# Performance work log

Measured on AMD Instinct MI355X. Metric: run time of the kernel, lower is better.

The kernel has to match this reference:

```python
import jax, jax.numpy as jnp
import numpy as np

D_MODEL = 1024
N_HEADS = 16
HEAD_DIM = D_MODEL // N_HEADS
SCALE = HEAD_DIM ** -0.5  # 0.125


def setup_inputs() -> dict:
    key = jax.random.key(0)
    k1, k2, k3, k4 = jax.random.split(key, 4)
    B, H, S, d = 2, N_HEADS, 2048, HEAD_DIM
    q = jax.random.normal(k1, (B, H, S, d), dtype=jnp.float32)
    k = jax.random.normal(k2, (B, H, d, S), dtype=jnp.float32)  # pre-transposed, as in torch.matmul(q, k)
    v = jax.random.normal(k3, (B, H, S, d), dtype=jnp.float32)
    prev = jax.random.normal(k4, (B, H, S, S), dtype=jnp.float32)
    return {"q": q, "k": k, "v": v, "prev": prev}


def reference(q, k, v, prev):
    # attn_scores = (q @ k) * scale + prev   (scores must be returned pre-softmax)
    attn_scores = jnp.einsum("bhsd,bhdt->bhst", q, k) * SCALE + prev
    attn_weights = jax.nn.softmax(attn_scores, axis=-1)
    # dropout p=0.0 -> identity (module default / eval)
    out = jnp.einsum("bhst,bhtd->bhsd", attn_weights, v)
    return (out, attn_scores)
```

## Files before the change

kernel.cpp:

```cpp
#include <hip/hip_runtime.h>
#include <hip/hip_fp16.h>


typedef _Float16 half8 __attribute__((ext_vector_type(8)));
typedef _Float16 half4v __attribute__((ext_vector_type(4)));
typedef float f32x4 __attribute__((ext_vector_type(4)));

constexpr int S_LEN = 2048;
constexpr int DHEAD = 64;
constexpr int BH_TOT = 32;
constexpr float SCALE = 0.125f;
constexpr float LOG2E = 1.4426950408889634f;
constexpr float M_FIX = 8.0f * LOG2E;

__global__ __launch_bounds__(256) void tconv(const float* __restrict__ in,
                                             _Float16* __restrict__ outp,
                                             int R, int C) {
    const int head = blockIdx.z;
    const int r0 = blockIdx.y * 64, c0 = blockIdx.x * 64;
    const float* src = in + (size_t)head * R * C;
    _Float16* dst = outp + (size_t)head * R * C;
    __shared__ _Float16 t[64][68];
    const int tx = threadIdx.x & 63;
    const int ty = threadIdx.x >> 6;
    #pragma unroll
    for (int i = 0; i < 16; ++i) {
        const int rr = ty + i * 4;
        t[tx][rr] = (_Float16)src[(size_t)(r0 + rr) * C + c0 + tx];
    }
    __syncthreads();
    const int cw = threadIdx.x >> 4;
    const int dx = (threadIdx.x & 15) * 4;
    #pragma unroll
    for (int i = 0; i < 4; ++i) {
        const int crow = cw + i * 16;
        half4v vv;
        #pragma unroll
        for (int j = 0; j < 4; ++j) vv[j] = t[crow][dx + j];
        *reinterpret_cast<half4v*>(&dst[(size_t)(c0 + crow) * R + r0 + dx]) = vv;
    }
}

__global__ __launch_bounds__(512, 4) void attn_fused(
    const float* __restrict__ q, const float* __restrict__ prev,
    const _Float16* __restrict__ k16t, const _Float16* __restrict__ v16t,
    float* __restrict__ out, float* __restrict__ scores)
{
    const int lane = threadIdx.x & 63;
    const int wave = threadIdx.x >> 6;
    const int lg = lane >> 4;
    const int lr = lane & 15;

    const int bid = blockIdx.x;
    const int swz = (bid & 7) * 64 + (bid >> 3);
    const int bh = swz >> 4;
    const int rb = swz & 15;
    const int i0 = rb * 128 + wave * 16;

    const float* qh = q + (size_t)bh * S_LEN * DHEAD;
    const float* ph = prev + (size_t)bh * S_LEN * S_LEN;
    float* sh = scores + (size_t)bh * S_LEN * S_LEN;
    float* oh = out + (size_t)bh * S_LEN * DHEAD;
    const _Float16* kt = k16t + (size_t)bh * S_LEN * DHEAD;
    const _Float16* vt = v16t + (size_t)bh * S_LEN * DHEAD;

    __shared__ __align__(16) _Float16 sbuf[2][4096];
    __shared__ __align__(16) _Float16 p_lds[8][16][40];

    const _Float16* sbase;
    size_t slaneoff;
    int smul;
    if (wave < 4) {
        const int r = wave * 8 + (lane >> 3);
        slaneoff = (size_t)r * DHEAD + (size_t)((((lane & 7) ^ (r & 7)) * 8));
        smul = DHEAD;
        sbase = kt;
    } else {
        const int d = (wave - 4) * 16 + (lane >> 2);
        slaneoff = (size_t)d * S_LEN + (size_t)((((lane & 3) ^ ((d >> 1) & 3)) * 8));
        smul = 1;
        sbase = vt;
    }
    _Float16* const dstA = &sbuf[0][wave * 512 + lane * 8];
    _Float16* const dstB = &sbuf[1][wave * 512 + lane * 8];

    half8 qa[2];
    {
        const float* qrow = qh + (size_t)(i0 + lr) * DHEAD + lg * 8;
        #pragma unroll
        for (int h = 0; h < 2; ++h) {
            half8 t;
            #pragma unroll
            for (int e = 0; e < 8; ++e) t[e] = (_Float16)qrow[h * 32 + e];
            qa[h] = t;
        }
    }

    f32x4 acc[4] = {};
    float lsum[4] = {0.f, 0.f, 0.f, 0.f};

    auto load_prev = [&](int jt, float (&P)[8]) {
        #pragma unroll
        for (int r = 0; r < 4; ++r) {
            const size_t rowoff = (size_t)(i0 + lg * 4 + r) * S_LEN + jt + lr;
            P[r * 2]     = ph[rowoff];
            P[r * 2 + 1] = ph[rowoff + 16];
        }
    };

    half8 R;

    auto step = [&](int t, float (&P)[8]) {
        const int b = t & 1;
        *reinterpret_cast<half8*>(b ? dstA : dstB) = R;
        const int tn = (t + 2 < 64) ? t + 2 : 63;
        R = *reinterpret_cast<const half8*>(sbase + (size_t)(tn * 32) * smul + slaneoff);

        const _Float16* kB = &sbuf[b][0];
        half8 kb[4];
        #pragma unroll
        for (int s = 0; s < 2; ++s) {
            const int r = s * 16 + lr;
            #pragma unroll
            for (int h = 0; h < 2; ++h)
                kb[s * 2 + h] = *reinterpret_cast<const half8*>(
                    kB + r * 64 + (((h * 4 + lg) ^ (lr & 7)) * 8));
        }
        f32x4 sacc[2] = {};
        sacc[0] = __builtin_amdgcn_mfma_f32_16x16x32_f16(qa[0], kb[0], sacc[0], 0, 0, 0);
        sacc[0] = __builtin_amdgcn_mfma_f32_16x16x32_f16(qa[1], kb[1], sacc[0], 0, 0, 0);
        sacc[1] = __builtin_amdgcn_mfma_f32_16x16x32_f16(qa[0], kb[2], sacc[1], 0, 0, 0);
        sacc[1] = __builtin_amdgcn_mfma_f32_16x16x32_f16(qa[1], kb[3], sacc[1], 0, 0, 0);

        const int jt = t * 32;
        #pragma unroll
        for (int r = 0; r < 4; ++r) {
            const int row = lg * 4 + r;
            const size_t rowoff = (size_t)(i0 + row) * S_LEN + jt + lr;
            const float a0 = fmaf(sacc[0][r], SCALE, P[r * 2]);
            const float a1 = fmaf(sacc[1][r], SCALE, P[r * 2 + 1]);
            sh[rowoff] = a0;
            sh[rowoff + 16] = a1;
            const float p0 = exp2f(fmaf(a0, LOG2E, -M_FIX));
            const float p1 = exp2f(fmaf(a1, LOG2E, -M_FIX));
            lsum[r] += p0 + p1;
            p_lds[wave][row][lr]      = (_Float16)p0;
            p_lds[wave][row][lr + 16] = (_Float16)p1;
        }
        load_prev(tn * 32, P);

        const half8 pa = *reinterpret_cast<const half8*>(&p_lds[wave][lr][lg * 8]);
        #pragma unroll
        for (int f = 0; f < 4; ++f) {
            const int d = f * 16 + lr;
            const half8 vb = *reinterpret_cast<const half8*>(
                kB + 2048 + d * 32 + ((lg ^ ((lr >> 1) & 3)) * 8));
            acc[f] = __builtin_amdgcn_mfma_f32_16x16x32_f16(pa, vb, acc[f], 0, 0, 0);
        }

        asm volatile("s_waitcnt lgkmcnt(0)" ::: "memory");
        __builtin_amdgcn_s_barrier();
        asm volatile("" ::: "memory");
    };

    float PA[8], PB[8];
    R = *reinterpret_cast<const half8*>(sbase + slaneoff);
    *reinterpret_cast<half8*>(dstA) = R;
    R = *reinterpret_cast<const half8*>(sbase + (size_t)32 * smul + slaneoff);
    load_prev(0, PA);
    load_prev(32, PB);
    asm volatile("s_waitcnt lgkmcnt(0)" ::: "memory");
    __builtin_amdgcn_s_barrier();
    asm volatile("" ::: "memory");

    for (int t = 0; t < 64; t += 2) {
        step(t, PA);
        step(t + 1, PB);
    }

    #pragma unroll
    for (int r = 0; r < 4; ++r) {
        float s = lsum[r];
        s += __shfl_xor(s, 1);
        s += __shfl_xor(s, 2);
        s += __shfl_xor(s, 4);
        s += __shfl_xor(s, 8);
        const float inv = 1.0f / s;
        const size_t o = (size_t)(i0 + lg * 4 + r) * DHEAD + lr;
        #pragma unroll
        for (int f = 0; f < 4; ++f)
            oh[o + f * 16] = acc[f][r] * inv;
    }
}

__global__ __launch_bounds__(256, 4) void attn_fallback(
    const float* __restrict__ q, const float* __restrict__ k,
    const float* __restrict__ v, const float* __restrict__ prev,
    float* __restrict__ out, float* __restrict__ scores)
{
    const int lane = threadIdx.x & 63;
    const int wave = threadIdx.x >> 6;
    const int lg = lane >> 4, lr = lane & 15;
    const int bh = blockIdx.x >> 5;
    const int rowblk = blockIdx.x & 31;
    const int i0 = rowblk * 64 + wave * 16;

    const float* qh = q + (size_t)bh * S_LEN * DHEAD;
    const float* kh = k + (size_t)bh * DHEAD * S_LEN;
    const float* vh = v + (size_t)bh * S_LEN * DHEAD;
    const float* ph = prev + (size_t)bh * S_LEN * S_LEN;
    float* sh = scores + (size_t)bh * S_LEN * S_LEN;
    float* oh = out + (size_t)bh * S_LEN * DHEAD;

    __shared__ __align__(16) _Float16 p_lds[4][16][40];

    half8 qa[2];
    {
        const float* qrow = qh + (size_t)(i0 + lr) * DHEAD + lg * 8;
        #pragma unroll
        for (int h = 0; h < 2; ++h) {
            half8 t;
            #pragma unroll
            for (int e = 0; e < 8; ++e) t[e] = (_Float16)qrow[h * 32 + e];
            qa[h] = t;
        }
    }
    f32x4 acc[4] = {};
    float lsum[4] = {0.f, 0.f, 0.f, 0.f};

    for (int jt = 0; jt < S_LEN; jt += 32) {
        half8 kb[4], vb[4];
        #pragma unroll
        for (int h = 0; h < 2; ++h)
            #pragma unroll
            for (int s = 0; s < 2; ++s) {
                const float* kp = kh + (size_t)(h * 32 + lg * 8) * S_LEN + jt + s * 16 + lr;
                half8 t;
                #pragma unroll
                for (int e = 0; e < 8; ++e) t[e] = (_Float16)kp[(size_t)e * S_LEN];
                kb[s * 2 + h] = t;
            }
        #pragma unroll
        for (int f = 0; f < 4; ++f) {
            const float* vp = vh + (size_t)(jt + lg * 8) * DHEAD + f * 16 + lr;
            half8 t;
            #pragma unroll
            for (int e = 0; e < 8; ++e) t[e] = (_Float16)vp[(size_t)e * DHEAD];
            vb[f] = t;
        }
        f32x4 sacc[2] = {};
        sacc[0] = __builtin_amdgcn_mfma_f32_16x16x32_f16(qa[0], kb[0], sacc[0], 0, 0, 0);
        sacc[0] = __builtin_amdgcn_mfma_f32_16x16x32_f16(qa[1], kb[1], sacc[0], 0, 0, 0);
        sacc[1] = __builtin_amdgcn_mfma_f32_16x16x32_f16(qa[0], kb[2], sacc[1], 0, 0, 0);
        sacc[1] = __builtin_amdgcn_mfma_f32_16x16x32_f16(qa[1], kb[3], sacc[1], 0, 0, 0);
        #pragma unroll
        for (int r = 0; r < 4; ++r) {
            const size_t rowoff = (size_t)(i0 + lg * 4 + r) * S_LEN + jt + lr;
            const float a0 = fmaf(sacc[0][r], SCALE, ph[rowoff]);
            const float a1 = fmaf(sacc[1][r], SCALE, ph[rowoff + 16]);
            sh[rowoff] = a0;
            sh[rowoff + 16] = a1;
            const float p0 = exp2f(fmaf(a0, LOG2E, -M_FIX));
            const float p1 = exp2f(fmaf(a1, LOG2E, -M_FIX));
            lsum[r] += p0 + p1;
            p_lds[wave][lg * 4 + r][lr]      = (_Float16)p0;
            p_lds[wave][lg * 4 + r][lr + 16] = (_Float16)p1;
        }
        const half8 pa = *reinterpret_cast<const half8*>(&p_lds[wave][lr][lg * 8]);
        #pragma unroll
        for (int f = 0; f < 4; ++f)
            acc[f] = __builtin_amdgcn_mfma_f32_16x16x32_f16(pa, vb[f], acc[f], 0, 0, 0);
    }
    #pragma unroll
    for (int r = 0; r < 4; ++r) {
        float s = lsum[r];
        s += __shfl_xor(s, 1);
        s += __shfl_xor(s, 2);
        s += __shfl_xor(s, 4);
        s += __shfl_xor(s, 8);
        const float inv = 1.0f / s;
        const size_t o = (size_t)(i0 + lg * 4 + r) * DHEAD + lr;
        #pragma unroll
        for (int f = 0; f < 4; ++f)
            oh[o + f * 16] = acc[f][r] * inv;
    }
}

extern "C" void kernel_launch(void* const* d_in, const int* in_sizes, int n_in,
                              void* d_out, int out_size, void* d_ws, size_t ws_size,
                              hipStream_t stream) {
    const float* q    = (const float*)d_in[0];
    const float* k    = (const float*)d_in[1];
    const float* v    = (const float*)d_in[2];
    const float* prev = (const float*)d_in[3];
    float* out = (float*)d_out;
    float* scores = out + (size_t)BH_TOT * S_LEN * DHEAD;

    const size_t elems = (size_t)BH_TOT * S_LEN * DHEAD;
    const size_t need = 2 * elems * sizeof(_Float16);

    if (d_ws != nullptr && ws_size >= need) {
        _Float16* k16t = (_Float16*)d_ws;
        _Float16* v16t = k16t + elems;
        tconv<<<dim3(S_LEN / 64, DHEAD / 64, BH_TOT), 256, 0, stream>>>(k, k16t, DHEAD, S_LEN);
        tconv<<<dim3(DHEAD / 64, S_LEN / 64, BH_TOT), 256, 0, stream>>>(v, v16t, S_LEN, DHEAD);
        attn_fused<<<dim3(512), dim3(512), 0, stream>>>(q, prev, k16t, v16t, out, scores);
    } else {
        attn_fallback<<<dim3(1024), dim3(256), 0, stream>>>(q, k, v, prev, out, scores);
    }
}
```

Baseline: 310.7 us.

## Double key tile width to 64 columns per pipeline step

Widens each step's key/value tile from 32 to 64 columns, halving the number of steps and barriers. All 512 threads now stage both K and V tiles instead of splitting waves between them, and each thread prefetches 16 prev values instead of 8. This is meant to cut barrier and loop overhead per unit of work, at the cost of doubled LDS and more registers, which may lower occupancy under launch_bounds(512,4).

```diff
diff --git a/kernel.cpp b/kernel.cpp
--- a/kernel.cpp
+++ b/kernel.cpp
@@ -46,8 +46,9 @@
     const _Float16* __restrict__ k16t, const _Float16* __restrict__ v16t,
     float* __restrict__ out, float* __restrict__ scores)
 {
-    const int lane = threadIdx.x & 63;
-    const int wave = threadIdx.x >> 6;
+    const int tid = threadIdx.x;
+    const int lane = tid & 63;
+    const int wave = tid >> 6;
     const int lg = lane >> 4;
     const int lr = lane & 15;
 
@@ -64,25 +65,15 @@
     const _Float16* kt = k16t + (size_t)bh * S_LEN * DHEAD;
     const _Float16* vt = v16t + (size_t)bh * S_LEN * DHEAD;
 
-    __shared__ __align__(16) _Float16 sbuf[2][4096];
-    __shared__ __align__(16) _Float16 p_lds[8][16][40];
-
-    const _Float16* sbase;
-    size_t slaneoff;
-    int smul;
-    if (wave < 4) {
-        const int r = wave * 8 + (lane >> 3);
-        slaneoff = (size_t)r * DHEAD + (size_t)((((lane & 7) ^ (r & 7)) * 8));
-        smul = DHEAD;
-        sbase = kt;
-    } else {
-        const int d = (wave - 4) * 16 + (lane >> 2);
-        slaneoff = (size_t)d * S_LEN + (size_t)((((lane & 3) ^ ((d >> 1) & 3)) * 8));
-        smul = 1;
-        sbase = vt;
-    }
-    _Float16* const dstA = &sbuf[0][wave * 512 + lane * 8];
-    _Float16* const dstB = &sbuf[1][wave * 512 + lane * 8];
+    __shared__ __align__(16) _Float16 sbuf[2][8192];
+    __shared__ __align__(16) _Float16 p_lds[8][16][72];
+
+    const int sr = tid >> 3;
+    const int s8 = tid & 7;
+    const size_t srcKoff = (size_t)sr * DHEAD + (size_t)((s8 ^ (sr & 7)) * 8);
+    const size_t srcVoff = (size_t)sr * S_LEN + (size_t)((s8 ^ (sr & 7)) * 8);
+    _Float16* const dK[2] = {&sbuf[0][tid * 8], &sbuf[1][tid * 8]};
+    _Float16* const dV[2] = {&sbuf[0][4096 + tid * 8], &sbuf[1][4096 + tid * 8]};
 
     half8 qa[2];
     {
@@ -99,63 +90,63 @@
     f32x4 acc[4] = {};
     float lsum[4] = {0.f, 0.f, 0.f, 0.f};
 
-    auto load_prev = [&](int jt, float (&P)[8]) {
+    auto load_prev = [&](int jt, float (&P)[16]) {
         #pragma unroll
         for (int r = 0; r < 4; ++r) {
             const size_t rowoff = (size_t)(i0 + lg * 4 + r) * S_LEN + jt + lr;
-            P[r * 2]     = ph[rowoff];
-            P[r * 2 + 1] = ph[rowoff + 16];
+            #pragma unroll
+            for (int s = 0; s < 4; ++s)
+                P[r * 4 + s] = ph[rowoff + s * 16];
         }
     };
 
-    half8 R;
-
-    auto step = [&](int t, float (&P)[8]) {
+    half8 RK, RV;
+
+    auto step = [&](int t, float (&P)[16]) {
         const int b = t & 1;
-        *reinterpret_cast<half8*>(b ? dstA : dstB) = R;
-        const int tn = (t + 2 < 64) ? t + 2 : 63;
-        R = *reinterpret_cast<const half8*>(sbase + (size_t)(tn * 32) * smul + slaneoff);
+        *reinterpret_cast<half8*>(dK[b ^ 1]) = RK;
+        *reinterpret_cast<half8*>(dV[b ^ 1]) = RV;
+        const int tn = (t + 2 < 32) ? t + 2 : 31;
+        RK = *reinterpret_cast<const half8*>(kt + (size_t)(tn * 64) * DHEAD + srcKoff);
+        RV = *reinterpret_cast<const half8*>(vt + (size_t)(tn * 64) + srcVoff);
 
         const _Float16* kB = &sbuf[b][0];
-        half8 kb[4];
-        #pragma unroll
-        for (int s = 0; s < 2; ++s) {
+        const int jt = t * 64;
+
+        #pragma unroll
+        for (int s = 0; s < 4; ++s) {
             const int r = s * 16 + lr;
-            #pragma unroll
-            for (int h = 0; h < 2; ++h)
-                kb[s * 2 + h] = *reinterpret_cast<const half8*>(
+            f32x4 sacc = {};
+            #pragma unroll
+            for (int h = 0; h < 2; ++h) {
+                const half8 kb = *reinterpret_cast<const half8*>(
                     kB + r * 64 + (((h * 4 + lg) ^ (lr & 7)) * 8));
-        }
-        f32x4 sacc[2] = {};
-        sacc[0] = __builtin_amdgcn_mfma_f32_16x16x32_f16(qa[0], kb[0], sacc[0], 0, 0, 0);
-        sacc[0] = __builtin_amdgcn_mfma_f32_16x16x32_f16(qa[1], kb[1], sacc[0], 0, 0, 0);
-        sacc[1] = __builtin_amdgcn_mfma_f32_16x16x32_f16(qa[0], kb[2], sacc[1], 0, 0, 0);
-        sacc[1] = __builtin_amdgcn_mfma_f32_16x16x32_f16(qa[1], kb[3], sacc[1], 0, 0, 0);
-
-        const int jt = t * 32;
-        #pragma unroll
-        for (int r = 0; r < 4; ++r) {
-            const int row = lg * 4 + r;
-            const size_t rowoff = (size_t)(i0 + row) * S_LEN + jt + lr;
-            const float a0 = fmaf(sacc[0][r], SCALE, P[r * 2]);
-            const float a1 = fmaf(sacc[1][r], SCALE, P[r * 2 + 1]);
-            sh[rowoff] = a0;
-            sh[rowoff + 16] = a1;
-            const float p0 = exp2f(fmaf(a0, LOG2E, -M_FIX));
-            const float p1 = exp2f(fmaf(a1, LOG2E, -M_FIX));
-            lsum[r] += p0 + p1;
-            p_lds[wave][row][lr]      = (_Float16)p0;
-            p_lds[wave][row][lr + 16] = (_Float16)p1;
-        }
-        load_prev(tn * 32, P);
-
-        const half8 pa = *reinterpret_cast<const half8*>(&p_lds[wave][lr][lg * 8]);
-        #pragma unroll
-        for (int f = 0; f < 4; ++f) {
-            const int d = f * 16 + lr;
-            const half8 vb = *reinterpret_cast<const half8*>(
-                kB + 2048 + d * 32 + ((lg ^ ((lr >> 1) & 3)) * 8));
-            acc[f] = __builtin_amdgcn_mfma_f32_16x16x32_f16(pa, vb, acc[f], 0, 0, 0);
+                sacc = __builtin_amdgcn_mfma_f32_16x16x32_f16(qa[h], kb, sacc, 0, 0, 0);
+            }
+            #pragma unroll
+            for (int rr = 0; rr < 4; ++rr) {
+                const int row = lg * 4 + rr;
+                const float a = fmaf(sacc[rr], SCALE, P[rr * 4 + s]);
+                sh[(size_t)(i0 + row) * S_LEN + jt + s * 16 + lr] = a;
+                const float p = exp2f(fmaf(a, LOG2E, -M_FIX));
+                lsum[rr] += p;
+                p_lds[wave][row][s * 16 + lr] = (_Float16)p;
+            }
+        }
+
+        load_prev(tn * 64, P);
+
+        #pragma unroll
+        for (int ks = 0; ks < 2; ++ks) {
+            const half8 pa = *reinterpret_cast<const half8*>(
+                &p_lds[wave][lr][ks * 32 + lg * 8]);
+            #pragma unroll
+            for (int f = 0; f < 4; ++f) {
+                const int d = f * 16 + lr;
+                const half8 vb = *reinterpret_cast<const half8*>(
+                    kB + 4096 + d * 64 + (((ks * 4 + lg) ^ (lr & 7)) * 8));
+                acc[f] = __builtin_amdgcn_mfma_f32_16x16x32_f16(pa, vb, acc[f], 0, 0, 0);
+            }
         }
 
         asm volatile("s_waitcnt lgkmcnt(0)" ::: "memory");
@@ -163,17 +154,20 @@
         asm volatile("" ::: "memory");
     };
 
-    float PA[8], PB[8];
-    R = *reinterpret_cast<const half8*>(sbase + slaneoff);
-    *reinterpret_cast<half8*>(dstA) = R;
-    R = *reinterpret_cast<const half8*>(sbase + (size_t)32 * smul + slaneoff);
+    float PA[16], PB[16];
+    RK = *reinterpret_cast<const half8*>(kt + srcKoff);
+    RV = *reinterpret_cast<const half8*>(vt + srcVoff);
+    *reinterpret_cast<half8*>(dK[0]) = RK;
+    *reinterpret_cast<half8*>(dV[0]) = RV;
+    RK = *reinterpret_cast<const half8*>(kt + (size_t)64 * DHEAD + srcKoff);
+    RV = *reinterpret_cast<const half8*>(vt + (size_t)64 + srcVoff);
     load_prev(0, PA);
-    load_prev(32, PB);
+    load_prev(64, PB);
     asm volatile("s_waitcnt lgkmcnt(0)" ::: "memory");
     __builtin_amdgcn_s_barrier();
     asm volatile("" ::: "memory");
 
-    for (int t = 0; t < 64; t += 2) {
+    for (int t = 0; t < 32; t += 2) {
         step(t, PA);
         step(t + 1, PB);
     }
```

After: 331.5 us. 1.07x slower.

## Halve attention block to 4 waves, share K/V staging, add MFMA priority

Applied to the files above, without the earlier changes.

Reduces each workgroup from 8 waves covering 128 query rows to 4 waves covering 64 rows, launching twice as many blocks. Every thread now stages both a K and a V fragment instead of splitting those roles across waves, and the block swizzle is updated to match. MFMA sections are wrapped in s_setprio raises so the matrix work gets issue priority over competing memory waves. Each K/V tile is now loaded by twice as many blocks, doubling L2 reads of K/V, while finer blocks aim to improve occupancy, load balance and barrier cost.

```diff
diff --git a/kernel.cpp b/kernel.cpp
--- a/kernel.cpp
+++ b/kernel.cpp
@@ -41,21 +41,22 @@
     }
 }
 
-__global__ __launch_bounds__(512, 4) void attn_fused(
+__global__ __launch_bounds__(256, 4) void attn_fused(
     const float* __restrict__ q, const float* __restrict__ prev,
     const _Float16* __restrict__ k16t, const _Float16* __restrict__ v16t,
     float* __restrict__ out, float* __restrict__ scores)
 {
-    const int lane = threadIdx.x & 63;
-    const int wave = threadIdx.x >> 6;
+    const int tid = threadIdx.x;
+    const int lane = tid & 63;
+    const int wave = tid >> 6;
     const int lg = lane >> 4;
     const int lr = lane & 15;
 
     const int bid = blockIdx.x;
-    const int swz = (bid & 7) * 64 + (bid >> 3);
-    const int bh = swz >> 4;
-    const int rb = swz & 15;
-    const int i0 = rb * 128 + wave * 16;
+    const int swz = (bid & 7) * 128 + (bid >> 3);
+    const int bh = swz >> 5;
+    const int rb = swz & 31;
+    const int i0 = rb * 64 + wave * 16;
 
     const float* qh = q + (size_t)bh * S_LEN * DHEAD;
     const float* ph = prev + (size_t)bh * S_LEN * S_LEN;
@@ -65,24 +66,18 @@
     const _Float16* vt = v16t + (size_t)bh * S_LEN * DHEAD;
 
     __shared__ __align__(16) _Float16 sbuf[2][4096];
-    __shared__ __align__(16) _Float16 p_lds[8][16][40];
-
-    const _Float16* sbase;
-    size_t slaneoff;
-    int smul;
-    if (wave < 4) {
-        const int r = wave * 8 + (lane >> 3);
-        slaneoff = (size_t)r * DHEAD + (size_t)((((lane & 7) ^ (r & 7)) * 8));
-        smul = DHEAD;
-        sbase = kt;
-    } else {
-        const int d = (wave - 4) * 16 + (lane >> 2);
-        slaneoff = (size_t)d * S_LEN + (size_t)((((lane & 3) ^ ((d >> 1) & 3)) * 8));
-        smul = 1;
-        sbase = vt;
-    }
-    _Float16* const dstA = &sbuf[0][wave * 512 + lane * 8];
-    _Float16* const dstB = &sbuf[1][wave * 512 + lane * 8];
+    __shared__ __align__(16) _Float16 p_lds[4][16][40];
+
+    const int sr = tid >> 3;
+    const int s8 = tid & 7;
+    const size_t srcKoff = (size_t)sr * DHEAD + (size_t)((s8 ^ (sr & 7)) * 8);
+    const int vd = tid >> 2;
+    const int v4 = tid & 3;
+    const size_t srcVoff = (size_t)vd * S_LEN + (size_t)(((v4 ^ ((vd >> 1) & 3)) * 8));
+    _Float16* const dKA = &sbuf[0][tid * 8];
+    _Float16* const dKB = &sbuf[1][tid * 8];
+    _Float16* const dVA = &sbuf[0][2048 + tid * 8];
+    _Float16* const dVB = &sbuf[1][2048 + tid * 8];
 
     half8 qa[2];
     {
@@ -108,13 +103,15 @@
         }
     };
 
-    half8 R;
+    half8 RK, RV;
 
     auto step = [&](int t, float (&P)[8]) {
         const int b = t & 1;
-        *reinterpret_cast<half8*>(b ? dstA : dstB) = R;
+        *reinterpret_cast<half8*>(b ? dKA : dKB) = RK;
+        *reinterpret_cast<half8*>(b ? dVA : dVB) = RV;
         const int tn = (t + 2 < 64) ? t + 2 : 63;
-        R = *reinterpret_cast<const half8*>(sbase + (size_t)(tn * 32) * smul + slaneoff);
+        RK = *reinterpret_cast<const half8*>(kt + (size_t)(tn * 32) * DHEAD + srcKoff);
+        RV = *reinterpret_cast<const half8*>(vt + (size_t)(tn * 32) + srcVoff);
 
         const _Float16* kB = &sbuf[b][0];
         half8 kb[4];
@@ -127,10 +124,12 @@
                     kB + r * 64 + (((h * 4 + lg) ^ (lr & 7)) * 8));
         }
         f32x4 sacc[2] = {};
+        __builtin_amdgcn_s_setprio(1);
         sacc[0] = __builtin_amdgcn_mfma_f32_16x16x32_f16(qa[0], kb[0], sacc[0], 0, 0, 0);
         sacc[0] = __builtin_amdgcn_mfma_f32_16x16x32_f16(qa[1], kb[1], sacc[0], 0, 0, 0);
         sacc[1] = __builtin_amdgcn_mfma_f32_16x16x32_f16(qa[0], kb[2], sacc[1], 0, 0, 0);
         sacc[1] = __builtin_amdgcn_mfma_f32_16x16x32_f16(qa[1], kb[3], sacc[1], 0, 0, 0);
+        __builtin_amdgcn_s_setprio(0);
 
         const int jt = t * 32;
         #pragma unroll
@@ -150,6 +149,7 @@
         load_prev(tn * 32, P);
 
         const half8 pa = *reinterpret_cast<const half8*>(&p_lds[wave][lr][lg * 8]);
+        __builtin_amdgcn_s_setprio(1);
         #pragma unroll
         for (int f = 0; f < 4; ++f) {
             const int d = f * 16 + lr;
@@ -157,6 +157,7 @@
                 kB + 2048 + d * 32 + ((lg ^ ((lr >> 1) & 3)) * 8));
             acc[f] = __builtin_amdgcn_mfma_f32_16x16x32_f16(pa, vb, acc[f], 0, 0, 0);
         }
+        __builtin_amdgcn_s_setprio(0);
 
         asm volatile("s_waitcnt lgkmcnt(0)" ::: "memory");
         __builtin_amdgcn_s_barrier();
@@ -164,9 +165,12 @@
     };
 
     float PA[8], PB[8];
-    R = *reinterpret_cast<const half8*>(sbase + slaneoff);
-    *reinterpret_cast<half8*>(dstA) = R;
-    R = *reinterpret_cast<const half8*>(sbase + (size_t)32 * smul + slaneoff);
+    RK = *reinterpret_cast<const half8*>(kt + srcKoff);
+    RV = *reinterpret_cast<const half8*>(vt + srcVoff);
+    *reinterpret_cast<half8*>(dKA) = RK;
+    *reinterpret_cast<half8*>(dVA) = RV;
+    RK = *reinterpret_cast<const half8*>(kt + (size_t)32 * DHEAD + srcKoff);
+    RV = *reinterpret_cast<const half8*>(vt + (size_t)32 + srcVoff);
     load_prev(0, PA);
     load_prev(32, PB);
     asm volatile("s_waitcnt lgkmcnt(0)" ::: "memory");
@@ -304,7 +308,7 @@
         _Float16* v16t = k16t + elems;
         tconv<<<dim3(S_LEN / 64, DHEAD / 64, BH_TOT), 256, 0, stream>>>(k, k16t, DHEAD, S_LEN);
         tconv<<<dim3(DHEAD / 64, S_LEN / 64, BH_TOT), 256, 0, stream>>>(v, v16t, S_LEN, DHEAD);
-        attn_fused<<<dim3(512), dim3(512), 0, stream>>>(q, prev, k16t, v16t, out, scores);
+        attn_fused<<<dim3(1024), dim3(256), 0, stream>>>(q, prev, k16t, v16t, out, scores);
     } else {
         attn_fallback<<<dim3(1024), dim3(256), 0, stream>>>(q, k, v, prev, out, scores);
     }
```

Measured after the change: 283.4 us. 8.8% less time.
